# Kernel tuning notes

Hardware: AMD Instinct MI355X
Metric: run time of the kernel (lower is better)

## Reference

```python
import jax, jax.numpy as jnp
import numpy as np

N_BATCH, D_FEAT, N_CLASSES = 96, 64, 21
MARGIN = 0.3


def setup_inputs() -> dict:
    key = jax.random.key(0)
    k1, k2, k3 = jax.random.split(key, 3)
    logits = jax.random.normal(k1, (N_BATCH, D_FEAT), dtype=jnp.float32)
    feat2 = jax.random.normal(k2, (N_BATCH, D_FEAT), dtype=jnp.float32)
    labels = (jax.random.uniform(k3, (N_BATCH, N_CLASSES)) < 0.3).astype(jnp.float32)
    return {"logits": logits, "labels": labels, "feat2": feat2}


def reference(logits, labels, feat2):
    """Dense-mask formulation of QuadrupletMarginMiner (defaults:
    margin=0.3, type_of_quadruplets='all', what_is_hard='one').

    Instead of a data-dependent list of quadruplets, returns a boolean
    tensor valid[i, j, k, n] that is True exactly for the quadruplets the
    torch module would return (same set, dense encoding).
    """
    n = labels.shape[0]
    eps = 1e-12

    # --- label structure ------------------------------------------------
    s = (labels @ labels.T) > 0                      # share-a-label matrix
    diffs = ~s                                       # torch: sames ^ 1 (pre diag fill)
    sames = s & ~jnp.eye(n, dtype=bool)              # fill_diagonal_(0)
    jk_triu = jnp.triu(jnp.ones((n, n), dtype=bool), k=1)  # strict j < k

    # valid (I, J, K) triples: AP1 & AP2 & j<k   -> [n, n, n]
    triple = sames[:, :, None] & sames[:, None, :] & jk_triu[None, :, :]
    # attach every negative N: diffs[i, n]        -> [n, n, n, n]
    quad = triple[:, :, :, None] & diffs[:, None, None, :]

    # --- distances (negative cosine similarity) ---------------------------
    xn = logits / jnp.maximum(jnp.linalg.norm(logits, axis=1, keepdims=True), eps)
    yn = feat2 / jnp.maximum(jnp.linalg.norm(feat2, axis=1, keepdims=True), eps)
    mat = -(xn @ yn.T)                               # [n, n]

    # margin_p[i, p, neg] = mat[i, neg] - mat[i, p]  (p stands for J or K)
    margin_pn = mat[:, None, :] - mat[:, :, None]    # [i, p, neg]
    viol = margin_pn <= MARGIN                       # [i, p, neg] bool

    # 'all' quadruplets + 'one' hardness: (margin1 <= m) | (margin2 <= m)
    cond = viol[:, :, None, :] | viol[:, None, :, :]  # [i, j, k, neg]

    return quad & cond
```

## Files before the change

### kernel.cpp

```cpp
#include <hip/hip_runtime.h>
#include <math.h>

#define NB 96
#define NB2 (NB * NB)
#define DFEAT 64
#define NCLS 21
#define MARGIN 0.3

typedef int i4 __attribute__((ext_vector_type(4)));

__global__ void precompute_kernel(const float* __restrict__ logits,
                                  const float* __restrict__ labels,
                                  const float* __restrict__ feat2,
                                  double* __restrict__ mat,
                                  double* __restrict__ thr,
                                  unsigned char* __restrict__ share) {
    int gid = blockIdx.x * blockDim.x + threadIdx.x;
    if (gid >= NB2) return;
    int i = gid / NB;
    int j = gid - i * NB;

    const float* xi = logits + i * DFEAT;
    const float* yj = feat2 + j * DFEAT;
    double nx = 0.0, ny = 0.0, dot = 0.0;
#pragma unroll
    for (int d = 0; d < DFEAT; ++d) {
        double a = (double)xi[d];
        double b = (double)yj[d];
        nx += a * a;
        ny += b * b;
        dot += a * b;
    }
    nx = fmax(sqrt(nx), 1e-12);
    ny = fmax(sqrt(ny), 1e-12);
    double m = -(dot / (nx * ny));
    mat[gid] = m;
    thr[gid] = MARGIN + m;

    const float* li = labels + i * NCLS;
    const float* lj = labels + j * NCLS;
    float ldot = 0.f;
#pragma unroll
    for (int c = 0; c < NCLS; ++c) ldot += li[c] * lj[c];
    share[gid] = (ldot > 0.f) ? 1 : 0;
}

__global__ __launch_bounds__(256) void quad_kernel(const double* __restrict__ mat,
                                                   const double* __restrict__ thr,
                                                   const unsigned char* __restrict__ share,
                                                   int* __restrict__ out) {
    const int bid = blockIdx.x;
    const int i = bid / NB;
    const int j = bid - i * NB;
    const int tid = threadIdx.x;

    __shared__ double smat[NB];
    __shared__ double sthr[NB];
    __shared__ unsigned char svalid[NB];

    if (tid < NB) {
        unsigned char s = share[i * NB + tid];
        double m = mat[i * NB + tid];
        smat[tid] = s ? 1e300 : m;
        sthr[tid] = thr[i * NB + tid];
        svalid[tid] = (s && tid != i) ? 1 : 0;
    }
    __syncthreads();

    const bool sames_ij = (svalid[j] != 0);
    const double thr_ij = sthr[j];
    i4* outp = (i4*)(out + (size_t)bid * (size_t)(NB * NB));

#pragma unroll
    for (int r = 0; r < 9; ++r) {
        int c = r * 256 + tid;
        int k = c / 24;
        int q = c - k * 24;
        i4 v = (i4)(0);
        if (sames_ij && svalid[k] && (j < k)) {
            double t = fmax(thr_ij, sthr[k]);
            int n0 = q * 4;
            v.x = (smat[n0 + 0] <= t) ? 1 : 0;
            v.y = (smat[n0 + 1] <= t) ? 1 : 0;
            v.z = (smat[n0 + 2] <= t) ? 1 : 0;
            v.w = (smat[n0 + 3] <= t) ? 1 : 0;
        }
        __builtin_nontemporal_store(v, &outp[c]);
    }
}

extern "C" void kernel_launch(void* const* d_in, const int* in_sizes, int n_in,
                              void* d_out, int out_size, void* d_ws, size_t ws_size,
                              hipStream_t stream) {
    const float* logits = (const float*)d_in[0];
    const float* labels = (const float*)d_in[1];
    const float* feat2  = (const float*)d_in[2];
    int* out = (int*)d_out;

    double* mat = (double*)d_ws;
    double* thr = mat + NB2;
    unsigned char* share = (unsigned char*)(thr + NB2);

    precompute_kernel<<<(NB2 + 255) / 256, 256, 0, stream>>>(logits, labels, feat2,
                                                             mat, thr, share);
    quad_kernel<<<NB2, 256, 0, stream>>>(mat, thr, share, out);
}
```

Before: 342.6 us.

## Fuse distance/label precompute into quad kernel with per-block row recompute

Removes the separate precompute kernel and workspace round-trip: each block recomputes row i of cosine distances and label-sharing for all 96 negatives using 4 lanes per entry with shuffle reductions. The output loop is restructured to 384 threads, where each thread keeps its four negative distances in registers and writes 6 k-rows. This cuts one launch and the global mat/thr/share traffic, at the cost of redundant recomputation of the row in every one of the 9216 blocks. The kernel is dominated by writing the large output, so the effect depends mostly on the store pattern.

Result: no change. 339.5 us (-0.9%).

```diff
diff --git a/kernel.cpp b/kernel.cpp
--- a/kernel.cpp
+++ b/kernel.cpp
@@ -9,99 +9,87 @@
 
 typedef int i4 __attribute__((ext_vector_type(4)));
 
-__global__ void precompute_kernel(const float* __restrict__ logits,
-                                  const float* __restrict__ labels,
-                                  const float* __restrict__ feat2,
-                                  double* __restrict__ mat,
-                                  double* __restrict__ thr,
-                                  unsigned char* __restrict__ share) {
-    int gid = blockIdx.x * blockDim.x + threadIdx.x;
-    if (gid >= NB2) return;
-    int i = gid / NB;
-    int j = gid - i * NB;
+__global__ __launch_bounds__(384) void fused_quad_kernel(
+    const float* __restrict__ logits,
+    const float* __restrict__ labels,
+    const float* __restrict__ feat2,
+    int* __restrict__ out) {
+  const int bid = blockIdx.x;
+  const int i = bid / NB;
+  const int j = bid - i * NB;
+  const int tid = threadIdx.x;
 
-    const float* xi = logits + i * DFEAT;
-    const float* yj = feat2 + j * DFEAT;
-    double nx = 0.0, ny = 0.0, dot = 0.0;
+  __shared__ double smat[NB];
+  __shared__ double sthr[NB];
+  __shared__ unsigned char svalid[NB];
+
+  {
+    const int n = tid >> 2;
+    const int l4 = tid & 3;
+    const float* xi = logits + i * DFEAT + l4 * 16;
+    const float* yn = feat2 + n * DFEAT + l4 * 16;
+    double dot = 0.0, nx = 0.0, ny = 0.0;
 #pragma unroll
-    for (int d = 0; d < DFEAT; ++d) {
-        double a = (double)xi[d];
-        double b = (double)yj[d];
-        nx += a * a;
-        ny += b * b;
-        dot += a * b;
+    for (int d = 0; d < 16; ++d) {
+      double a = (double)xi[d];
+      double b = (double)yn[d];
+      dot += a * b;
+      nx += a * a;
+      ny += b * b;
     }
-    nx = fmax(sqrt(nx), 1e-12);
-    ny = fmax(sqrt(ny), 1e-12);
-    double m = -(dot / (nx * ny));
-    mat[gid] = m;
-    thr[gid] = MARGIN + m;
+    dot += __shfl_xor(dot, 1); nx += __shfl_xor(nx, 1); ny += __shfl_xor(ny, 1);
+    dot += __shfl_xor(dot, 2); nx += __shfl_xor(nx, 2); ny += __shfl_xor(ny, 2);
+    if (l4 == 0) {
+      nx = fmax(sqrt(nx), 1e-12);
+      ny = fmax(sqrt(ny), 1e-12);
+      double m = -(dot / (nx * ny));
+      const float* li = labels + i * NCLS;
+      const float* ln = labels + n * NCLS;
+      float ld = 0.f;
+#pragma unroll
+      for (int c = 0; c < NCLS; ++c) ld += li[c] * ln[c];
+      const bool share = (ld > 0.f);
+      smat[n] = share ? 1e300 : m;
+      sthr[n] = MARGIN + m;
+      svalid[n] = (share && n != i) ? 1 : 0;
+    }
+  }
+  __syncthreads();
 
-    const float* li = labels + i * NCLS;
-    const float* lj = labels + j * NCLS;
-    float ldot = 0.f;
-#pragma unroll
-    for (int c = 0; c < NCLS; ++c) ldot += li[c] * lj[c];
-    share[gid] = (ldot > 0.f) ? 1 : 0;
-}
+  const bool sames_ij = (svalid[j] != 0);
+  const double thr_ij = sthr[j];
+  i4* outp = (i4*)(out + (size_t)bid * (size_t)NB2);
 
-__global__ __launch_bounds__(256) void quad_kernel(const double* __restrict__ mat,
-                                                   const double* __restrict__ thr,
-                                                   const unsigned char* __restrict__ share,
-                                                   int* __restrict__ out) {
-    const int bid = blockIdx.x;
-    const int i = bid / NB;
-    const int j = bid - i * NB;
-    const int tid = threadIdx.x;
-
-    __shared__ double smat[NB];
-    __shared__ double sthr[NB];
-    __shared__ unsigned char svalid[NB];
-
-    if (tid < NB) {
-        unsigned char s = share[i * NB + tid];
-        double m = mat[i * NB + tid];
-        smat[tid] = s ? 1e300 : m;
-        sthr[tid] = thr[i * NB + tid];
-        svalid[tid] = (s && tid != i) ? 1 : 0;
-    }
-    __syncthreads();
-
-    const bool sames_ij = (svalid[j] != 0);
-    const double thr_ij = sthr[j];
-    i4* outp = (i4*)(out + (size_t)bid * (size_t)(NB * NB));
+  const int q = tid % 24;
+  const int kg = tid / 24;
+  const int n0 = q * 4;
+  const double d0 = smat[n0 + 0];
+  const double d1 = smat[n0 + 1];
+  const double d2 = smat[n0 + 2];
+  const double d3 = smat[n0 + 3];
 
 #pragma unroll
-    for (int r = 0; r < 9; ++r) {
-        int c = r * 256 + tid;
-        int k = c / 24;
-        int q = c - k * 24;
-        i4 v = (i4)(0);
-        if (sames_ij && svalid[k] && (j < k)) {
-            double t = fmax(thr_ij, sthr[k]);
-            int n0 = q * 4;
-            v.x = (smat[n0 + 0] <= t) ? 1 : 0;
-            v.y = (smat[n0 + 1] <= t) ? 1 : 0;
-            v.z = (smat[n0 + 2] <= t) ? 1 : 0;
-            v.w = (smat[n0 + 3] <= t) ? 1 : 0;
-        }
-        __builtin_nontemporal_store(v, &outp[c]);
+  for (int r = 0; r < 6; ++r) {
+    const int k = kg * 6 + r;
+    i4 v = (i4)(0);
+    if (sames_ij && svalid[k] && (j < k)) {
+      const double t = fmax(thr_ij, sthr[k]);
+      v.x = (d0 <= t) ? 1 : 0;
+      v.y = (d1 <= t) ? 1 : 0;
+      v.z = (d2 <= t) ? 1 : 0;
+      v.w = (d3 <= t) ? 1 : 0;
     }
+    __builtin_nontemporal_store(v, &outp[k * 24 + q]);
+  }
 }
 
 extern "C" void kernel_launch(void* const* d_in, const int* in_sizes, int n_in,
                               void* d_out, int out_size, void* d_ws, size_t ws_size,
                               hipStream_t stream) {
-    const float* logits = (const float*)d_in[0];
-    const float* labels = (const float*)d_in[1];
-    const float* feat2  = (const float*)d_in[2];
-    int* out = (int*)d_out;
+  const float* logits = (const float*)d_in[0];
+  const float* labels = (const float*)d_in[1];
+  const float* feat2  = (const float*)d_in[2];
+  int* out = (int*)d_out;
 
-    double* mat = (double*)d_ws;
-    double* thr = mat + NB2;
-    unsigned char* share = (unsigned char*)(thr + NB2);
-
-    precompute_kernel<<<(NB2 + 255) / 256, 256, 0, stream>>>(logits, labels, feat2,
-                                                             mat, thr, share);
-    quad_kernel<<<NB2, 256, 0, stream>>>(mat, thr, share, out);
+  fused_quad_kernel<<<NB2, 384, 0, stream>>>(logits, labels, feat2, out);
 }
```
